# Kernel optimization log

Measured on AMD Instinct MI355X. Metric: run time of the kernel, lower is better.

Reference implementation:

```python
import jax, jax.numpy as jnp
import numpy as np

B = 8192      # batch
E = 16        # n_experts
D = 128       # per-expert input dim (equal for all experts)
U = 256       # units
F = 256       # feature_dim (gating input)
G = 4         # n_gates
K = 6         # hard-coded top-k in the original call()
TEMP = 0.01   # hard-coded softmax temperature
LEAKY_SLOPE = 0.2  # keras leaky_relu default negative slope


def setup_inputs() -> dict:
    key = jax.random.key(0)
    ks = jax.random.split(key, 5)
    return {
        "inputs": jax.random.normal(ks[0], (B, E * D), dtype=jnp.float32),
        "feature_input": jax.random.normal(ks[1], (B, F), dtype=jnp.float32),
        # stacked per-expert kernels (equal dims -> one [E, D, U] tensor)
        "expert_kernels": jax.random.normal(ks[2], (E, D, U), dtype=jnp.float32) * 0.05,
        "expert_biases": jnp.zeros((E, U), dtype=jnp.float32),
        "gating_kernels": jax.random.normal(ks[3], (G, F, E), dtype=jnp.float32) * 0.1,
        "gating_biases": jnp.zeros((G, E), dtype=jnp.float32),
        "global_weights": jnp.ones((E,), dtype=jnp.float32),
    }


def reference(inputs, feature_input, expert_kernels, expert_biases,
              gating_kernels, gating_biases, global_weights):
    # ---- per-expert dense + bias + LeakyReLU (tf.split loop -> batched einsum) ----
    x = inputs.reshape(B, E, D)                                   # [B, E, D]
    eo = jnp.einsum('bed,edu->bue', x, expert_kernels)            # [B, U, E]
    eo = eo + expert_biases.T[None, :, :]                         # bias per expert
    expert_outputs = jax.nn.leaky_relu(eo, LEAKY_SLOPE)           # [B, U, E]

    # ---- gating: dense + bias + ReLU, scaled by global_weights ----
    g = jnp.einsum('bf,gfe->bge', feature_input, gating_kernels)  # [B, G, E]
    g = jax.nn.relu(g + gating_biases[None, :, :]) * global_weights

    # sharp softmax over experts, then top-k selection
    p = jax.nn.softmax(g / TEMP, axis=-1)                         # [B, G, E]
    top_v, top_i = jax.lax.top_k(p, K)                            # [B, G, K]

    # gather selected expert outputs: [B, G, U, K]
    sel = jnp.take_along_axis(expert_outputs[:, None, :, :],
                              top_i[:, :, None, :], axis=-1)

    # renormalize top-k values with another sharp softmax, weighted combine
    w = jax.nn.softmax(top_v / TEMP, axis=-1)                     # [B, G, K]
    out = jnp.einsum('bguk,bgk->bgu', sel, w)                     # [B, G, U]
    concat_output = out.reshape(B, G * U)                         # concat over gates
    return concat_output, expert_outputs
```

## Files before the change

### kernel.cpp

```cpp
#include <hip/hip_runtime.h>
#include <stdint.h>

#define NB 8192
#define NE 16
#define ND 128
#define NU 256
#define NF 256
#define NG 4
#define NK 6
#define ITEMP_LOG2E 144.26950408889634f

typedef short short4v __attribute__((ext_vector_type(4)));
typedef short short8v __attribute__((ext_vector_type(8)));
typedef float float4v __attribute__((ext_vector_type(4)));

__device__ __forceinline__ short f2bf(float x) {
  uint32_t u = __builtin_bit_cast(uint32_t, x);
  u += 0x7FFFu + ((u >> 16) & 1u);
  return (short)(u >> 16);
}

__global__ __launch_bounds__(256) void prep_kernel(
    const float* __restrict__ ek,
    const float* __restrict__ feat,
    const float* __restrict__ gk,
    const float* __restrict__ gbias,
    const float* __restrict__ gw,
    short* __restrict__ pb,
    float* __restrict__ wd)
{
  int bid = blockIdx.x, tid = threadIdx.x;
  if (bid < 256) {
    int gid = (bid << 8) | tid;
    int lane = gid & 63, ut = (gid >> 6) & 15, ks = (gid >> 10) & 3, e = gid >> 12;
    int krow = ks * 32 + ((lane >> 4) * 8);
    int ucol = ut * 16 + (lane & 15);
    const float* src = ek + (size_t)(e * 128 + krow) * 256 + ucol;
    short8v v;
#pragma unroll
    for (int j = 0; j < 8; ++j) v[j] = f2bf(src[(size_t)j * 256]);
    size_t widx = (((size_t)ut * 16 + e) * 4 + ks) * 64 + lane;
    *(short8v*)(pb + widx * 8) = v;
  } else {
    int w = tid >> 6, lane = tid & 63;
    int rb = w * 8;
    int gate = lane >> 4, e = lane & 15;
    float gwv = gw[e];
    float bias = gbias[gate * 16 + e];
    const float* gkp = gk + (size_t)gate * (NF * NE) + e;
    size_t b0 = (size_t)(bid - 256) * 32 + rb;
    const float* fb = feat + b0 * 256;
    float acc[8];
#pragma unroll
    for (int i = 0; i < 8; ++i) acc[i] = bias;
#pragma unroll 1
    for (int f0 = 0; f0 < NF; f0 += 16) {
      float gv[16];
#pragma unroll
      for (int j = 0; j < 16; ++j) gv[j] = gkp[(f0 + j) * 16];
#pragma unroll
      for (int j = 0; j < 16; j += 4) {
#pragma unroll
        for (int i = 0; i < 8; ++i) {
          float4v fv = *(const float4v*)(fb + i * 256 + f0 + j);
          acc[i] = fmaf(fv[0], gv[j + 0], acc[i]);
          acc[i] = fmaf(fv[1], gv[j + 1], acc[i]);
          acc[i] = fmaf(fv[2], gv[j + 2], acc[i]);
          acc[i] = fmaf(fv[3], gv[j + 3], acc[i]);
        }
      }
    }
#pragma unroll 1
    for (int i = 0; i < 8; ++i) {
      float v = acc[i] > 0.f ? acc[i] : 0.f;
      v *= gwv;
      float m = v;
#pragma unroll
      for (int off = 1; off < 16; off <<= 1) m = fmaxf(m, __shfl_xor(m, off, 16));
      float ex = exp2f((v - m) * ITEMP_LOG2E);
      float s = ex;
#pragma unroll
      for (int off = 1; off < 16; off <<= 1) s += __shfl_xor(s, off, 16);
      float pr = ex / s;
      float cur = pr;
      float topv[NK]; int topi[NK];
#pragma unroll
      for (int r = 0; r < NK; ++r) {
        float mv = cur;
#pragma unroll
        for (int off = 1; off < 16; off <<= 1) mv = fmaxf(mv, __shfl_xor(mv, off, 16));
        int cand = (cur == mv) ? e : 16;
#pragma unroll
        for (int off = 1; off < 16; off <<= 1) cand = min(cand, __shfl_xor(cand, off, 16));
        topv[r] = mv; topi[r] = cand;
        if (e == cand) cur = -1.f;
      }
      float wv[NK], wsum = 0.f;
#pragma unroll
      for (int r = 0; r < NK; ++r) {
        wv[r] = exp2f((topv[r] - topv[0]) * ITEMP_LOG2E);
        wsum += wv[r];
      }
      float inv = 1.f / wsum;
      float wdv = 0.f;
#pragma unroll
      for (int r = 0; r < NK; ++r) wdv = (topi[r] == e) ? wv[r] * inv : wdv;
      wd[(b0 + i) * 64 + lane] = wdv;
    }
  }
}

#define APITCH 2056

__global__ __launch_bounds__(512, 4) void gemm_kernel(
    const float* __restrict__ x,
    const float* __restrict__ eb,
    const short* __restrict__ pb,
    float* __restrict__ outeo)
{
  __shared__ __align__(16) short ash[16 * APITCH];
  __shared__ __align__(16) float stg[8 * 256];
  int bt = blockIdx.x, tid = threadIdx.x;
  int w = tid >> 6, lane = tid & 63;

  {
    const float4v* s = (const float4v*)(x + (size_t)bt * 16 * 2048);
    float4v buf[8];
#pragma unroll
    for (int c = 0; c < 2; ++c) {
#pragma unroll
      for (int k = 0; k < 8; ++k)
        buf[k] = __builtin_nontemporal_load(s + tid + (c * 8 + k) * 512);
#pragma unroll
      for (int k = 0; k < 8; ++k) {
        int idx = tid + (c * 8 + k) * 512;
        int row = idx >> 9, colf = (idx & 511) << 2;
        short4v sv;
        sv[0] = f2bf(buf[k][0]); sv[1] = f2bf(buf[k][1]);
        sv[2] = f2bf(buf[k][2]); sv[3] = f2bf(buf[k][3]);
        *(short4v*)&ash[row * APITCH + colf] = sv;
      }
    }
  }
  __syncthreads();

  int utq = w & 3, th = w >> 2;
  int q = lane >> 4, col = lane & 15;
  int am = lane & 15;
  const short8v* pbv = (const short8v*)pb;
  float* ws = stg + w * 256;
  size_t bb = (size_t)bt * 16;
  int arow = am * APITCH;

#pragma unroll 1
  for (int tl = 0; tl < 2; ++tl) {
    int ut = utq * 4 + th * 2 + tl;
    const short8v* bp = pbv + (size_t)ut * 4096;
    float4v acc[16];
    float4v zero = {0.f, 0.f, 0.f, 0.f};
#pragma unroll
    for (int e = 0; e < 16; ++e) acc[e] = zero;
    short8v bA[4], bB[4];
#pragma unroll
    for (int ks = 0; ks < 4; ++ks) bA[ks] = bp[ks * 64 + lane];
#pragma unroll
    for (int e = 0; e < 16; e += 2) {
#pragma unroll
      for (int ks = 0; ks < 4; ++ks) bB[ks] = bp[(e + 1) * 256 + ks * 64 + lane];
#pragma unroll
      for (int ks = 0; ks < 4; ++ks) {
        short8v a = *(const short8v*)&ash[arow + e * 128 + ks * 32 + q * 8];
        acc[e] = __builtin_amdgcn_mfma_f32_16x16x32_bf16(a, bA[ks], acc[e], 0, 0, 0);
      }
      if (e + 2 < 16) {
#pragma unroll
        for (int ks = 0; ks < 4; ++ks) bA[ks] = bp[(e + 2) * 256 + ks * 64 + lane];
      }
#pragma unroll
      for (int ks = 0; ks < 4; ++ks) {
        short8v a = *(const short8v*)&ash[arow + (e + 1) * 128 + ks * 32 + q * 8];
        acc[e + 1] = __builtin_amdgcn_mfma_f32_16x16x32_bf16(a, bB[ks], acc[e + 1], 0, 0, 0);
      }
    }
    float v[16][4];
#pragma unroll
    for (int e = 0; e < 16; ++e) {
      float bv = eb[e * 256 + ut * 16 + col];
#pragma unroll
      for (int r = 0; r < 4; ++r) {
        float z = acc[e][r] + bv;
        v[e][r] = z > 0.f ? z : 0.2f * z;
      }
    }
#pragma unroll
    for (int r = 0; r < 4; ++r) {
#pragma unroll
      for (int qq = 0; qq < 4; ++qq) {
        if (q == qq) {
#pragma unroll
          for (int c = 0; c < 4; ++c) {
            float4v o = {v[4 * c + 0][r], v[4 * c + 1][r], v[4 * c + 2][r], v[4 * c + 3][r]};
            *(float4v*)(ws + (c * 16 + col) * 4) = o;
          }
        }
        __builtin_amdgcn_wave_barrier();
        {
          size_t b = bb + (size_t)(qq * 4 + r);
          float4v val = *(const float4v*)(ws + lane * 4);
          float* dst = outeo + b * 4096 + (size_t)ut * 256 + (lane & 15) * 16 + (lane >> 4) * 4;
          *(float4v*)dst = val;
        }
        __builtin_amdgcn_wave_barrier();
      }
    }
  }
}

__global__ __launch_bounds__(256) void combine_kernel(
    const float* __restrict__ eo,
    const float* __restrict__ wd,
    float* __restrict__ outcat)
{
  __shared__ float wl[256];
  int bt = blockIdx.x, tid = threadIdx.x;
  wl[tid] = wd[(size_t)bt * 256 + tid];
  __syncthreads();
#pragma unroll 1
  for (int i = 0; i < 4; ++i) {
    size_t b = (size_t)bt * 4 + i;
    const float4v* ep = (const float4v*)(eo + b * 4096 + (size_t)tid * 16);
    float4v e0 = ep[0], e1 = ep[1], e2 = ep[2], e3 = ep[3];
    const float* wp = wl + i * 64;
#pragma unroll
    for (int g = 0; g < 4; ++g) {
      const float* wg = wp + g * 16;
      float s = 0.f;
      s = fmaf(wg[0],  e0[0], s); s = fmaf(wg[1],  e0[1], s);
      s = fmaf(wg[2],  e0[2], s); s = fmaf(wg[3],  e0[3], s);
      s = fmaf(wg[4],  e1[0], s); s = fmaf(wg[5],  e1[1], s);
      s = fmaf(wg[6],  e1[2], s); s = fmaf(wg[7],  e1[3], s);
      s = fmaf(wg[8],  e2[0], s); s = fmaf(wg[9],  e2[1], s);
      s = fmaf(wg[10], e2[2], s); s = fmaf(wg[11], e2[3], s);
      s = fmaf(wg[12], e3[0], s); s = fmaf(wg[13], e3[1], s);
      s = fmaf(wg[14], e3[2], s); s = fmaf(wg[15], e3[3], s);
      outcat[b * 1024 + g * 256 + tid] = s;
    }
  }
}

extern "C" void kernel_launch(void* const* d_in, const int* in_sizes, int n_in,
                              void* d_out, int out_size, void* d_ws, size_t ws_size,
                              hipStream_t stream) {
  const float* x     = (const float*)d_in[0];
  const float* feat  = (const float*)d_in[1];
  const float* ek    = (const float*)d_in[2];
  const float* eb    = (const float*)d_in[3];
  const float* gk    = (const float*)d_in[4];
  const float* gbias = (const float*)d_in[5];
  const float* gw    = (const float*)d_in[6];
  float* out = (float*)d_out;
  float* outcat = out;
  float* outeo  = out + (size_t)NB * NG * NU;
  float* wd  = (float*)d_ws;
  short* pbf = (short*)((char*)d_ws + (size_t)NB * NG * NE * 4);

  prep_kernel<<<512, 256, 0, stream>>>(ek, feat, gk, gbias, gw, pbf, wd);
  gemm_kernel<<<512, 512, 0, stream>>>(x, eb, pbf, outeo);
  combine_kernel<<<2048, 256, 0, stream>>>(outeo, wd, outcat);
}
```

Before: 323.0 us.

## Fuse gated top-k combine into expert GEMM epilogue, drop combine kernel

Removes the separate combine kernel. Each GEMM block now loads its 16 rows of dense gate weights into shared memory and computes the per-gate weighted sum over experts from the accumulator registers in the epilogue. The combined output is written directly, so the large expert-output tensor no longer has to be read back from global memory and one launch is saved. It also changes the A-tile pitch and adds some shared memory and registers, which may affect occupancy.

```diff
diff --git a/kernel.cpp b/kernel.cpp
--- a/kernel.cpp
+++ b/kernel.cpp
@@ -110,19 +110,27 @@
   }
 }
 
-#define APITCH 2056
-
-__global__ __launch_bounds__(512, 4) void gemm_kernel(
+#define APITCH 2064
+#define WPITCH 64
+
+__global__ __launch_bounds__(512, 4) void moe_kernel(
     const float* __restrict__ x,
     const float* __restrict__ eb,
     const short* __restrict__ pb,
-    float* __restrict__ outeo)
+    const float* __restrict__ wd,
+    float* __restrict__ out)
 {
   __shared__ __align__(16) short ash[16 * APITCH];
   __shared__ __align__(16) float stg[8 * 256];
+  __shared__ __align__(16) float wsh[16 * WPITCH];
   int bt = blockIdx.x, tid = threadIdx.x;
   int w = tid >> 6, lane = tid & 63;
 
+#pragma unroll
+  for (int k = 0; k < 2; ++k) {
+    int i = tid + k * 512;
+    wsh[i] = wd[(size_t)bt * 1024 + i];
+  }
   {
     const float4v* s = (const float4v*)(x + (size_t)bt * 16 * 2048);
     float4v buf[8];
@@ -147,10 +155,15 @@
   int utq = w & 3, th = w >> 2;
   int q = lane >> 4, col = lane & 15;
   int am = lane & 15;
+  float* outcat = out;
+  float* outeo = out + (size_t)NB * NG * NU;
   const short8v* pbv = (const short8v*)pb;
   float* ws = stg + w * 256;
   size_t bb = (size_t)bt * 16;
   int arow = am * APITCH;
+  int wrow = (q * 4) * WPITCH;
+
+  float csave[4][4];
 
 #pragma unroll 1
   for (int tl = 0; tl < 2; ++tl) {
@@ -213,37 +226,28 @@
         __builtin_amdgcn_wave_barrier();
       }
     }
-  }
-}
-
-__global__ __launch_bounds__(256) void combine_kernel(
-    const float* __restrict__ eo,
-    const float* __restrict__ wd,
-    float* __restrict__ outcat)
-{
-  __shared__ float wl[256];
-  int bt = blockIdx.x, tid = threadIdx.x;
-  wl[tid] = wd[(size_t)bt * 256 + tid];
-  __syncthreads();
-#pragma unroll 1
-  for (int i = 0; i < 4; ++i) {
-    size_t b = (size_t)bt * 4 + i;
-    const float4v* ep = (const float4v*)(eo + b * 4096 + (size_t)tid * 16);
-    float4v e0 = ep[0], e1 = ep[1], e2 = ep[2], e3 = ep[3];
-    const float* wp = wl + i * 64;
-#pragma unroll
-    for (int g = 0; g < 4; ++g) {
-      const float* wg = wp + g * 16;
-      float s = 0.f;
-      s = fmaf(wg[0],  e0[0], s); s = fmaf(wg[1],  e0[1], s);
-      s = fmaf(wg[2],  e0[2], s); s = fmaf(wg[3],  e0[3], s);
-      s = fmaf(wg[4],  e1[0], s); s = fmaf(wg[5],  e1[1], s);
-      s = fmaf(wg[6],  e1[2], s); s = fmaf(wg[7],  e1[3], s);
-      s = fmaf(wg[8],  e2[0], s); s = fmaf(wg[9],  e2[1], s);
-      s = fmaf(wg[10], e2[2], s); s = fmaf(wg[11], e2[3], s);
-      s = fmaf(wg[12], e3[0], s); s = fmaf(wg[13], e3[1], s);
-      s = fmaf(wg[14], e3[2], s); s = fmaf(wg[15], e3[3], s);
-      outcat[b * 1024 + g * 256 + tid] = s;
+#pragma unroll
+    for (int r = 0; r < 4; ++r) {
+      size_t b = bb + (size_t)(q * 4 + r);
+#pragma unroll
+      for (int g = 0; g < 4; ++g) {
+        float sacc = 0.f;
+#pragma unroll
+        for (int ec = 0; ec < 16; ec += 4) {
+          float4v wv = *(const float4v*)&wsh[wrow + r * WPITCH + g * 16 + ec];
+          sacc = fmaf(wv[0], v[ec][r], sacc);
+          sacc = fmaf(wv[1], v[ec + 1][r], sacc);
+          sacc = fmaf(wv[2], v[ec + 2][r], sacc);
+          sacc = fmaf(wv[3], v[ec + 3][r], sacc);
+        }
+        if (tl == 0) {
+          csave[r][g] = sacc;
+        } else {
+          float* cb = outcat + b * 1024 + g * 256 + (ut - 1) * 16 + col;
+          cb[0] = csave[r][g];
+          cb[16] = sacc;
+        }
+      }
     }
   }
 }
@@ -259,12 +263,9 @@
   const float* gbias = (const float*)d_in[5];
   const float* gw    = (const float*)d_in[6];
   float* out = (float*)d_out;
-  float* outcat = out;
-  float* outeo  = out + (size_t)NB * NG * NU;
   float* wd  = (float*)d_ws;
   short* pbf = (short*)((char*)d_ws + (size_t)NB * NG * NE * 4);
 
   prep_kernel<<<512, 256, 0, stream>>>(ek, feat, gk, gbias, gw, pbf, wd);
-  gemm_kernel<<<512, 512, 0, stream>>>(x, eb, pbf, outeo);
-  combine_kernel<<<2048, 256, 0, stream>>>(outeo, wd, outcat);
-}
+  moe_kernel<<<512, 512, 0, stream>>>(x, eb, pbf, wd, out);
+}
```

After: 331.1 us. 2.5% more time.
